# Kernel tuning notes

Measured on AMD Instinct MI355X. Metric: run time of the kernel, lower is better.

Reference implementation:

```python
import jax, jax.numpy as jnp
import numpy as np

B, N, IN, HD, NH, L, OUT = 256, 128, 9, 128, 8, 4, 60
DH = HD // NH
ALPHA = 0.6
EPS = 1e-5

def _ln(x, g, b):
    m = jnp.mean(x, axis=-1, keepdims=True)
    v = jnp.mean((x - m) ** 2, axis=-1, keepdims=True)
    return (x - m) * jax.lax.rsqrt(v + EPS) * g + b

def setup_inputs():
    key = jax.random.key(0)
    ks = jax.random.split(key, 30)
    p = lambda i, s: jax.random.normal(ks[i], s, jnp.float32) * 0.02
    strong = (jax.random.uniform(ks[25], (N, N)) < 0.15).astype(jnp.float32)
    strong = jnp.maximum(strong, jnp.eye(N, dtype=jnp.float32))  # self loops
    weak_mask = (jax.random.uniform(ks[26], (N, N)) < 0.10).astype(jnp.float32)
    return {
        'x': jax.random.normal(ks[0], (B, N, IN), jnp.float32),
        'conv_w': p(1, (HD, IN)), 'conv_b': p(2, (HD,)),
        'bn_gamma': jnp.ones((HD,), jnp.float32), 'bn_beta': jnp.zeros((HD,), jnp.float32),
        'bn_mean': jnp.zeros((HD,), jnp.float32), 'bn_var': jnp.ones((HD,), jnp.float32),
        'W': p(3, (L, HD, HD)), 'a_src': p(4, (L, NH, DH)), 'a_dst': p(5, (L, NH, DH)),
        'ln_g': jnp.ones((L, HD), jnp.float32), 'ln_b': jnp.zeros((L, HD), jnp.float32),
        'ffn_w1': p(6, (L, HD, 2 * HD)), 'ffn_b1': p(7, (L, 2 * HD)),
        'ffn_w2': p(8, (L, 2 * HD, HD)), 'ffn_b2': p(9, (L, HD)),
        'norm_g': jnp.ones((HD,), jnp.float32), 'norm_b': jnp.zeros((HD,), jnp.float32),
        'proj_w': p(10, (HD, HD)), 'proj_b': p(11, (HD,)),
        'head_w1': p(12, (HD, HD // 2)), 'head_b1': p(13, (HD // 2,)),
        'head_w2': p(14, (HD // 2, OUT)), 'head_b2': p(15, (OUT,)),
        'strong_adj': strong, 'weak_mask': weak_mask,
        'weak_param': p(16, (N, N)), 'edge_weight_adj': p(17, (N, N)),
    }

def reference(x, conv_w, conv_b, bn_gamma, bn_beta, bn_mean, bn_var, W, a_src, a_dst, ln_g, ln_b, ffn_w1, ffn_b1, ffn_w2, ffn_b2, norm_g, norm_b, proj_w, proj_b, head_w1, head_b1, head_w2, head_b2, strong_adj, weak_mask, weak_param, edge_weight_adj):
    # embedding: Conv1d(k=1) == per-node linear, then eval-mode BatchNorm1d + ReLU
    h = jnp.einsum('bni,oi->bno', x, conv_w) + conv_b  # [B,N,HD]
    h = (h - bn_mean) * jax.lax.rsqrt(bn_var + EPS) * bn_gamma + bn_beta
    h = jax.nn.relu(h)
    # weak adjacency: learnable gated edges, row-normalized (shared across layers)
    Aw = jax.nn.sigmoid(weak_param) * weak_mask
    Aw = Aw / (jnp.sum(Aw, axis=-1, keepdims=True) + EPS)  # [N,N]
    for i in range(L):
        res = h
        hp = jnp.einsum('bnd,de->bne', h, W[i]).reshape(B, N, NH, DH)
        s = jnp.einsum('bnhd,hd->bnh', hp, a_src[i])
        t = jnp.einsum('bnhd,hd->bnh', hp, a_dst[i])
        e = jax.nn.leaky_relu(s[:, :, None, :] + t[:, None, :, :], 0.2)  # [B,N,N,H]
        e = e + edge_weight_adj[None, :, :, None]  # learned per-edge bias
        e = jnp.where(strong_adj[None, :, :, None] > 0, e, jnp.float32(-1e9))
        att = jax.nn.softmax(e, axis=2)  # softmax over neighbors j
        strong_out = jnp.einsum('bijh,bjhd->bihd', att, hp)
        weak_out = jnp.einsum('ij,bjhd->bihd', Aw, hp)
        g = jax.nn.relu(ALPHA * strong_out + (1.0 - ALPHA) * weak_out).reshape(B, N, HD)
        g = _ln(g, ln_g[i], ln_b[i])
        g = jax.nn.relu(g @ ffn_w1[i] + ffn_b1[i]) @ ffn_w2[i] + ffn_b2[i]
        h = g + res
    h = _ln(h, norm_g, norm_b)
    h = h @ proj_w + proj_b
    h = jnp.mean(h, axis=1)  # mean-pool over nodes -> [B,HD]
    h = jax.nn.relu(h @ head_w1 + head_b1)
    return h @ head_w2 + head_b2  # [B,OUT]
```

## Files before the change

kernel.cpp:

```cpp
#include <hip/hip_runtime.h>
#include <hip/hip_bf16.h>

typedef __hip_bfloat16 bf16;
typedef unsigned short u16;
typedef __attribute__((ext_vector_type(8))) short bfrag;
typedef __attribute__((ext_vector_type(4))) float cfrag;

union BF { bfrag v; u16 u[8]; unsigned w[4]; };
union CF { cfrag v; float f[4]; };

#define MFMA(a,b,c) __builtin_amdgcn_mfma_f32_16x16x32_bf16(a,b,c,0,0,0)

#define BB   256
#define NN   128
#define IND  9
#define HDD  128
#define LLY  4
#define OUTD 60
#define LOG2E 1.44269504f
#define STR  136

__device__ __forceinline__ float b2f(bf16 v){ return __bfloat162float(v); }
__device__ __forceinline__ float u2f(u16 u){ return __uint_as_float(((unsigned)u) << 16); }
__device__ __forceinline__ u16 f2bf_bits(float f){
    unsigned u = __float_as_uint(f);
    return (u16)((u + 0x7FFFu + ((u >> 16) & 1u)) >> 16);
}
__device__ __forceinline__ unsigned pk2(float a, float b){
    union { __hip_bfloat162 h; unsigned u; } c;
    c.h = __float22bfloat162_rn(make_float2(a, b));
    return c.u;
}
__device__ __forceinline__ float wave_sum(float v){
    #pragma unroll
    for (int m = 32; m; m >>= 1) v += __shfl_xor(v, m, 64);
    return v;
}
__device__ __forceinline__ float ldin(const void* p, int i, bool isbf){
    return isbf ? b2f(((const bf16*)p)[i]) : ((const float*)p)[i];
}

struct SrcPtrs { const void* p[28]; };

__device__ const int NCV_OFF[19] = {0,1152,1280,1408,1536,1664,1792,2304,2816,3840,
                                    4352,4480,4608,20992,21120,29312,29376,33216,33276};
__device__ const int NCV_SRC[18] = {1,2,3,4,5,6,10,11,13,15,16,17,18,19,20,21,22,23};

__global__ __launch_bounds__(256) void k_prep(
    SrcPtrs S, float* __restrict__ pf,
    u16* __restrict__ WT, u16* __restrict__ w1T, u16* __restrict__ w2T,
    u16* __restrict__ WAb, u16* __restrict__ ew2, u16* __restrict__ Aw16,
    int* __restrict__ flagOut)
{
    __shared__ float tile[64][65];
    const unsigned* xw = (const unsigned*)S.p[0];
    int lane = threadIdx.x & 63;
    int cnt = 0;
    for (int i = lane; i < 512; i += 64) {
        float v = __uint_as_float((xw[i] & 0xFFFFu) << 16);
        if (!(fabsf(v) < 32.f)) cnt++;
    }
    bool isbf = wave_sum((float)cnt) < 16.f;
    if (blockIdx.x == 0 && threadIdx.x == 0) *flagOut = isbf ? 1 : 0;

    int blk = blockIdx.x, tid = threadIdx.x;
    if (blk < 131) {
        int idx = blk * 256 + tid;
        if (idx < 33276) {
            int y = 17;
            #pragma unroll 1
            for (int t = 1; t < 18; t++) if (idx < NCV_OFF[t]) { y = t - 1; break; }
            pf[idx] = ldin(S.p[NCV_SRC[y]], idx - NCV_OFF[y], isbf);
        }
    } else if (blk < 211) {
        const void* src; u16* dst; int K, N, k0, n0;
        if (blk < 147) {
            int t = blk - 131, l = t >> 2, tt = t & 3;
            src = (const char*)S.p[7] + (size_t)l * 16384 * (isbf ? 2 : 4);
            dst = WT + l * 16384; K = 128; N = 128; k0 = (tt >> 1) * 64; n0 = (tt & 1) * 64;
        } else if (blk < 179) {
            int t = blk - 147, l = t >> 3, tt = t & 7;
            src = (const char*)S.p[12] + (size_t)l * 32768 * (isbf ? 2 : 4);
            dst = w1T + l * 32768; K = 128; N = 256; k0 = (tt >> 2) * 64; n0 = (tt & 3) * 64;
        } else {
            int t = blk - 179, l = t >> 3, tt = t & 7;
            src = (const char*)S.p[14] + (size_t)l * 32768 * (isbf ? 2 : 4);
            dst = w2T + l * 32768; K = 256; N = 128; k0 = (tt & 3) * 64; n0 = (tt >> 2) * 64;
        }
        int ty = tid >> 6, tx = tid & 63;
        #pragma unroll 4
        for (int i = 0; i < 16; i++) {
            int row = ty * 16 + i;
            tile[row][tx] = ldin(src, (k0 + row) * N + n0 + tx, isbf);
        }
        __syncthreads();
        #pragma unroll 4
        for (int i = 0; i < 16; i++) {
            int row = ty * 16 + i;
            dst[(n0 + row) * K + k0 + tx] = f2bf_bits(tile[tx][row]);
        }
    } else if (blk < 243) {
        int j = (blk - 211) * 256 + tid;
        int l = j >> 11, r = j & 2047, n = r >> 7, k = r & 127;
        int h = n & 7;
        const void* ap = (n < 8) ? S.p[8] : S.p[9];
        float sacc = 0.f;
        #pragma unroll 1
        for (int d = 0; d < 16; d++)
            sacc += ldin(S.p[7], l * 16384 + k * 128 + h * 16 + d, isbf)
                  * ldin(ap, l * 128 + h * 16 + d, isbf);
        WAb[j] = f2bf_bits(sacc);
    } else if (blk < 307) {
        int j = (blk - 243) * 256 + tid;
        float sav = ldin(S.p[24], j, isbf);
        float ewv = ldin(S.p[27], j, isbf);
        ew2[j] = f2bf_bits(sav > 0.f ? ewv * LOG2E : -1e30f);
    } else {
        __shared__ float red[2];
        int i = blk - 307, j = tid & 127;
        float v = 0.f;
        if (tid < 128) {
            float wmv = ldin(S.p[25], i * 128 + j, isbf);
            float wpv = ldin(S.p[26], i * 128 + j, isbf);
            v = wmv / (1.f + __expf(-wpv));
            float sm = wave_sum(v);
            if ((tid & 63) == 0) red[tid >> 6] = sm;
        }
        __syncthreads();
        if (tid < 128) {
            float tot = red[0] + red[1];
            Aw16[i * 128 + j] = f2bf_bits(0.4f * v / (tot + 1e-5f));
        }
    }
}

#define LDSB (128*STR*2*2 + 128*132*4 + 2560*4)
__global__ __launch_bounds__(512, 2) void k_net(
    const void* __restrict__ xraw, const int* __restrict__ flag,
    const float* __restrict__ pf,
    const u16* __restrict__ WTg, const u16* __restrict__ WAbg,
    const u16* __restrict__ Awg, const u16* __restrict__ ew2g,
    const u16* __restrict__ w1Tg, const u16* __restrict__ w2Tg,
    void* __restrict__ outv)
{
    extern __shared__ __align__(16) char smem[];
    u16* U1 = (u16*)smem;
    u16* U2 = U1 + 128 * STR;
    float* hf32 = (float*)(U2 + 128 * STR);
    float* st2  = hf32 + 128 * 132;
    float* s2   = st2;
    u16*   t2u  = (u16*)(st2 + 1024);
    float* invb = st2 + 1536;

    const int b = blockIdx.x;
    const int tid = threadIdx.x, lane = tid & 63, wv = tid >> 6;
    const int l15 = lane & 15, kg = lane >> 4;
    const int wrow = wv * 16;
    const int arow = wrow + l15;
    const bool isbf = (*flag != 0);

    {
        float xr[4][IND];
        #pragma unroll
        for (int r = 0; r < 4; r++) {
            int bn = b * NN + wrow + kg * 4 + r;
            #pragma unroll
            for (int k = 0; k < IND; k++) xr[r][k] = ldin(xraw, bn * IND + k, isbf);
        }
        #pragma unroll 1
        for (int nt = 0; nt < 8; nt++) {
            int d = nt * 16 + l15;
            float cwreg[IND];
            #pragma unroll
            for (int k = 0; k < IND; k++) cwreg[k] = pf[d * IND + k];
            float scale = rsqrtf(pf[1664 + d] + 1e-5f) * pf[1280 + d];
            float bias  = pf[1408 + d] - pf[1536 + d] * scale;
            float cbd   = pf[1152 + d];
            #pragma unroll
            for (int r = 0; r < 4; r++) {
                float a = cbd;
                #pragma unroll
                for (int k = 0; k < IND; k++) a = fmaf(xr[r][k], cwreg[k], a);
                a = fmaxf(fmaf(a, scale, bias), 0.f);
                int row = wrow + kg * 4 + r;
                hf32[row * 132 + d] = a;
                U1[row * STR + d] = f2bf_bits(a);
            }
        }
    }

    #pragma unroll 1
    for (int l = 0; l < LLY; l++) {
        const u16* WT  = WTg  + l * 16384;
        const u16* WAb = WAbg + l * 2048;
        const u16* w1T = w1Tg + l * 32768;
        const u16* w2T = w2Tg + l * 32768;
        const float* fb1 = pf + 2816 + l * 256;
        const float* fb2 = pf + 3840 + l * 128;
        const float* lng = pf + 1792 + l * 128;
        const float* lnb = pf + 2304 + l * 128;

        __syncthreads();

        {
            CF acc[8], ast;
            #pragma unroll
            for (int r = 0; r < 4; r++) ast.f[r] = 0.f;
            #pragma unroll
            for (int nt = 0; nt < 8; nt++)
                #pragma unroll
                for (int r = 0; r < 4; r++) acc[nt].f[r] = 0.f;
            #pragma unroll
            for (int kk = 0; kk < 4; kk++) {
                bfrag af  = *(const bfrag*)&U1[arow * STR + kk*32 + kg*8];
                bfrag wab = *(const bfrag*)&WAb[l15 * 128 + kk*32 + kg*8];
                ast.v = MFMA(af, wab, ast.v);
                #pragma unroll
                for (int nt = 0; nt < 8; nt++) {
                    bfrag bw = *(const bfrag*)&WT[(nt*16 + l15) * 128 + kk*32 + kg*8];
                    acc[nt].v = MFMA(af, bw, acc[nt].v);
                }
            }
            #pragma unroll
            for (int nt = 0; nt < 8; nt++) {
                int col = nt*16 + l15;
                #pragma unroll
                for (int rp = 0; rp < 2; rp++) {
                    int row = wrow + kg*4 + rp*2;
                    *(unsigned*)&U2[col * STR + row] = pk2(acc[nt].f[rp*2], acc[nt].f[rp*2+1]);
                }
            }
            #pragma unroll
            for (int r = 0; r < 4; r++) {
                int node = wrow + kg*4 + r;
                float v = ast.f[r] * LOG2E;
                if (l15 < 8) s2[l15 * 128 + node] = v;
                else         t2u[(l15 - 8) * 128 + node] = f2bf_bits(v);
            }
        }
        __syncthreads();

        CF accS[8];
        #pragma unroll
        for (int nt = 0; nt < 8; nt++)
            #pragma unroll
            for (int r = 0; r < 4; r++) accS[nt].f[r] = 0.f;
        BF e2f[4];
        #pragma unroll
        for (int kk = 0; kk < 4; kk++)
            e2f[kk].v = *(const bfrag*)&ew2g[arow * 128 + kk*32 + kg*8];
        #pragma unroll 1
        for (int h = 0; h < 8; h++) {
            float sA = s2[h * 128 + arow];
            float sm = 0.f;
            #pragma unroll
            for (int kk = 0; kk < 4; kk++) {
                bfrag hb = *(const bfrag*)&U2[(h*16 + l15) * STR + kk*32 + kg*8];
                BF tb; tb.v = *(const bfrag*)&t2u[h * 128 + kk*32 + kg*8];
                BF pb;
                float p0[8];
                #pragma unroll
                for (int j = 0; j < 8; j++) {
                    float x2 = sA + u2f(tb.u[j]);
                    float lk = fmaxf(x2, 0.2f * x2);
                    float p = __builtin_amdgcn_exp2f(lk + u2f(e2f[kk].u[j]));
                    p0[j] = p; sm += p;
                }
                #pragma unroll
                for (int q = 0; q < 4; q++) pb.w[q] = pk2(p0[2*q], p0[2*q+1]);
                accS[h].v = MFMA(pb.v, hb, accS[h].v);
            }
            sm += __shfl_xor(sm, 16, 64);
            sm += __shfl_xor(sm, 32, 64);
            invb[h * 128 + arow] = 0.6f * __builtin_amdgcn_rcpf(sm);
        }
        #pragma unroll
        for (int h = 0; h < 8; h++) {
            const float4 iv = *(const float4*)&invb[h * 128 + wrow + kg*4];
            accS[h].f[0] *= iv.x; accS[h].f[1] *= iv.y;
            accS[h].f[2] *= iv.z; accS[h].f[3] *= iv.w;
        }

        #pragma unroll
        for (int kk = 0; kk < 4; kk++) {
            bfrag awf = *(const bfrag*)&Awg[arow * 128 + kk*32 + kg*8];
            #pragma unroll
            for (int nt = 0; nt < 8; nt++) {
                bfrag hb2 = *(const bfrag*)&U2[(nt*16 + l15) * STR + kk*32 + kg*8];
                accS[nt].v = MFMA(awf, hb2, accS[nt].v);
            }
        }

        #pragma unroll
        for (int r = 0; r < 4; r++) {
            float s1 = 0.f, sq = 0.f;
            #pragma unroll
            for (int nt = 0; nt < 8; nt++) {
                float x = fmaxf(accS[nt].f[r], 0.f);
                accS[nt].f[r] = x; s1 += x; sq = fmaf(x, x, sq);
            }
            #pragma unroll
            for (int m = 1; m <= 8; m <<= 1) { s1 += __shfl_xor(s1, m, 64); sq += __shfl_xor(sq, m, 64); }
            float mu = s1 * (1.f / 128.f);
            float var = sq * (1.f / 128.f) - mu * mu;
            float rs = rsqrtf(fmaxf(var, 0.f) + 1e-5f);
            #pragma unroll
            for (int nt = 0; nt < 8; nt++) {
                int col = nt*16 + l15;
                U1[(wrow + kg*4 + r) * STR + col] =
                    f2bf_bits(fmaf((accS[nt].f[r] - mu) * rs, lng[col], lnb[col]));
            }
        }

        __syncthreads();
        CF acc2[8];
        #pragma unroll
        for (int nt = 0; nt < 8; nt++)
            #pragma unroll
            for (int r = 0; r < 4; r++) acc2[nt].f[r] = 0.f;
        #pragma unroll 1
        for (int nh = 0; nh < 2; nh++) {
            CF a1[8];
            #pragma unroll
            for (int nt = 0; nt < 8; nt++)
                #pragma unroll
                for (int r = 0; r < 4; r++) a1[nt].f[r] = 0.f;
            #pragma unroll
            for (int kk = 0; kk < 4; kk++) {
                bfrag gf = *(const bfrag*)&U1[arow * STR + kk*32 + kg*8];
                #pragma unroll
                for (int nt = 0; nt < 8; nt++) {
                    bfrag wf = *(const bfrag*)&w1T[(nh*128 + nt*16 + l15) * 128 + kk*32 + kg*8];
                    a1[nt].v = MFMA(gf, wf, a1[nt].v);
                }
            }
            #pragma unroll
            for (int nt = 0; nt < 8; nt++) {
                int col = nt*16 + l15;
                float b1v = fb1[nh*128 + col];
                #pragma unroll
                for (int r = 0; r < 4; r++)
                    U2[(wrow + kg*4 + r) * STR + col] = f2bf_bits(fmaxf(a1[nt].f[r] + b1v, 0.f));
            }
            #pragma unroll
            for (int kk = 0; kk < 4; kk++) {
                bfrag hf = *(const bfrag*)&U2[arow * STR + kk*32 + kg*8];
                #pragma unroll
                for (int nt = 0; nt < 8; nt++) {
                    bfrag wf = *(const bfrag*)&w2T[(nt*16 + l15) * 256 + nh*128 + kk*32 + kg*8];
                    acc2[nt].v = MFMA(hf, wf, acc2[nt].v);
                }
            }
        }

        #pragma unroll
        for (int nt = 0; nt < 8; nt++) {
            int col = nt*16 + l15;
            float b2v = fb2[col];
            #pragma unroll
            for (int r = 0; r < 4; r++) {
                int row = wrow + kg*4 + r;
                float hv = hf32[row * 132 + col] + acc2[nt].f[r] + b2v;
                hf32[row * 132 + col] = hv;
                if (l < LLY - 1) U1[row * STR + col] = f2bf_bits(hv);
            }
        }
    }

    const float* ng = pf + 4352;
    const float* nb = pf + 4480;
    float pacc[8];
    #pragma unroll
    for (int nt = 0; nt < 8; nt++) pacc[nt] = 0.f;
    #pragma unroll
    for (int r = 0; r < 4; r++) {
        int row = wrow + kg*4 + r;
        float hvv[8];
        float s1 = 0.f, sq = 0.f;
        #pragma unroll
        for (int nt = 0; nt < 8; nt++) {
            float x = hf32[row * 132 + nt*16 + l15];
            hvv[nt] = x; s1 += x; sq = fmaf(x, x, sq);
        }
        #pragma unroll
        for (int m = 1; m <= 8; m <<= 1) { s1 += __shfl_xor(s1, m, 64); sq += __shfl_xor(sq, m, 64); }
        float mu = s1 * (1.f / 128.f);
        float var = sq * (1.f / 128.f) - mu * mu;
        float rs = rsqrtf(fmaxf(var, 0.f) + 1e-5f);
        #pragma unroll
        for (int nt = 0; nt < 8; nt++)
            pacc[nt] += fmaf((hvv[nt] - mu) * rs, ng[nt*16 + l15], nb[nt*16 + l15]);
    }
    #pragma unroll
    for (int nt = 0; nt < 8; nt++) {
        pacc[nt] += __shfl_xor(pacc[nt], 16, 64);
        pacc[nt] += __shfl_xor(pacc[nt], 32, 64);
    }
    __syncthreads();
    if (kg == 0) {
        #pragma unroll
        for (int nt = 0; nt < 8; nt++) st2[wv * 128 + nt*16 + l15] = pacc[nt];
    }
    __syncthreads();
    if (tid < 128) {
        float tot = 0.f;
        #pragma unroll
        for (int w = 0; w < 8; w++) tot += st2[w * 128 + tid];
        st2[1024 + tid] = tot * (1.f / 128.f);
    }
    __syncthreads();
    {
        int e = tid & 127, kq = tid >> 7;
        float a = 0.f;
        #pragma unroll 4
        for (int k = kq * 32; k < kq * 32 + 32; k++)
            a = fmaf(st2[1024 + k], pf[4608 + k * 128 + e], a);
        st2[1152 + kq * 128 + e] = a;
    }
    __syncthreads();
    if (tid < 128)
        st2[1664 + tid] = st2[1152 + tid] + st2[1280 + tid] + st2[1408 + tid] + st2[1536 + tid]
                        + pf[20992 + tid];
    __syncthreads();
    if (tid < 64) {
        float a1 = pf[29312 + tid];
        #pragma unroll 4
        for (int k = 0; k < 128; k++) a1 = fmaf(st2[1664 + k], pf[21120 + k * 64 + tid], a1);
        st2[1792 + tid] = fmaxf(a1, 0.f);
    }
    __syncthreads();
    if (tid < OUTD) {
        float a2 = pf[33216 + tid];
        #pragma unroll 4
        for (int k = 0; k < 64; k++) a2 = fmaf(st2[1792 + k], pf[29376 + k * OUTD + tid], a2);
        if (isbf) ((bf16*)outv)[b * OUTD + tid] = __float2bfloat16(a2);
        else      ((float*)outv)[b * OUTD + tid] = a2;
    }
}

extern "C" void kernel_launch(void* const* d_in, const int* in_sizes, int n_in,
                              void* d_out, int out_size, void* d_ws, size_t ws_size,
                              hipStream_t stream)
{
    float* ws = (float*)d_ws;
    float* pf = ws;
    int*   flag = (int*)(ws + 33280);
    u16* WT16   = (u16*)(ws + 33536);
    u16* w1T16  = WT16 + 65536;
    u16* w2T16  = w1T16 + 131072;
    u16* WAb16  = w2T16 + 131072;
    u16* Aw16   = WAb16 + 8192;
    u16* ew2p   = Aw16 + 16384;

    SrcPtrs S;
    for (int i = 0; i < 28; i++) S.p[i] = d_in[i];

    hipFuncSetAttribute((const void*)k_net,
                        hipFuncAttributeMaxDynamicSharedMemorySize, LDSB);

    k_prep<<<435, 256, 0, stream>>>(S, pf, WT16, w1T16, w2T16, WAb16, ew2p, Aw16, flag);
    k_net<<<BB, 512, LDSB, stream>>>(d_in[0], flag, pf,
                                     WT16, WAb16, Aw16, ew2p, w1T16, w2T16, d_out);
}
```

Measured before the change: 401.5 us.

## Split GEMMs into half-width passes and fold softmax normalization before MFMA

Splits the W projection and FFN first-layer GEMMs into two passes of four output tiles each, which reduces live accumulator registers. The weak-adjacency aggregation now runs before the attention loop. Each head's softmax probabilities are scaled by the reciprocal sum before the bf16 pack, which removes the invb LDS buffer and the per-head rescale pass. Launch bounds change from 2 blocks per CU to 1, so the compiler may use more registers, and scaling probabilities before bf16 conversion slightly changes rounding.

```diff
diff --git a/kernel.cpp b/kernel.cpp
--- a/kernel.cpp
+++ b/kernel.cpp
@@ -135,7 +135,7 @@
 }
 
 #define LDSB (128*STR*2*2 + 128*132*4 + 2560*4)
-__global__ __launch_bounds__(512, 2) void k_net(
+__global__ __launch_bounds__(512, 1) void k_net(
     const void* __restrict__ xraw, const int* __restrict__ flag,
     const float* __restrict__ pf,
     const u16* __restrict__ WTg, const u16* __restrict__ WAbg,
@@ -146,11 +146,10 @@
     extern __shared__ __align__(16) char smem[];
     u16* U1 = (u16*)smem;
     u16* U2 = U1 + 128 * STR;
-    float* hf32 = (float*)(U2 + 128 * STR);
-    float* st2  = hf32 + 128 * 132;
+    float* hres = (float*)(U2 + 128 * STR);
+    float* st2  = hres + 128 * 132;
     float* s2   = st2;
     u16*   t2u  = (u16*)(st2 + 1024);
-    float* invb = st2 + 1536;
 
     const int b = blockIdx.x;
     const int tid = threadIdx.x, lane = tid & 63, wv = tid >> 6;
@@ -183,7 +182,7 @@
                 for (int k = 0; k < IND; k++) a = fmaf(xr[r][k], cwreg[k], a);
                 a = fmaxf(fmaf(a, scale, bias), 0.f);
                 int row = wrow + kg * 4 + r;
-                hf32[row * 132 + d] = a;
+                hres[row * 132 + d] = a;
                 U1[row * STR + d] = f2bf_bits(a);
             }
         }
@@ -202,40 +201,45 @@
 
         __syncthreads();
 
-        {
-            CF acc[8], ast;
+        #pragma unroll 1
+        for (int pass = 0; pass < 2; pass++) {
+            CF acc[4], ast;
+            #pragma unroll
+            for (int q = 0; q < 4; q++)
+                #pragma unroll
+                for (int r = 0; r < 4; r++) acc[q].f[r] = 0.f;
             #pragma unroll
             for (int r = 0; r < 4; r++) ast.f[r] = 0.f;
             #pragma unroll
-            for (int nt = 0; nt < 8; nt++)
-                #pragma unroll
-                for (int r = 0; r < 4; r++) acc[nt].f[r] = 0.f;
-            #pragma unroll
             for (int kk = 0; kk < 4; kk++) {
-                bfrag af  = *(const bfrag*)&U1[arow * STR + kk*32 + kg*8];
-                bfrag wab = *(const bfrag*)&WAb[l15 * 128 + kk*32 + kg*8];
-                ast.v = MFMA(af, wab, ast.v);
-                #pragma unroll
-                for (int nt = 0; nt < 8; nt++) {
-                    bfrag bw = *(const bfrag*)&WT[(nt*16 + l15) * 128 + kk*32 + kg*8];
-                    acc[nt].v = MFMA(af, bw, acc[nt].v);
-                }
-            }
-            #pragma unroll
-            for (int nt = 0; nt < 8; nt++) {
-                int col = nt*16 + l15;
+                bfrag af = *(const bfrag*)&U1[arow * STR + kk*32 + kg*8];
+                if (pass == 0) {
+                    bfrag wab = *(const bfrag*)&WAb[l15 * 128 + kk*32 + kg*8];
+                    ast.v = MFMA(af, wab, ast.v);
+                }
+                #pragma unroll
+                for (int q = 0; q < 4; q++) {
+                    bfrag bw = *(const bfrag*)&WT[((pass*4+q)*16 + l15) * 128 + kk*32 + kg*8];
+                    acc[q].v = MFMA(af, bw, acc[q].v);
+                }
+            }
+            #pragma unroll
+            for (int q = 0; q < 4; q++) {
+                int col = (pass*4+q)*16 + l15;
                 #pragma unroll
                 for (int rp = 0; rp < 2; rp++) {
                     int row = wrow + kg*4 + rp*2;
-                    *(unsigned*)&U2[col * STR + row] = pk2(acc[nt].f[rp*2], acc[nt].f[rp*2+1]);
-                }
-            }
-            #pragma unroll
-            for (int r = 0; r < 4; r++) {
-                int node = wrow + kg*4 + r;
-                float v = ast.f[r] * LOG2E;
-                if (l15 < 8) s2[l15 * 128 + node] = v;
-                else         t2u[(l15 - 8) * 128 + node] = f2bf_bits(v);
+                    *(unsigned*)&U2[col * STR + row] = pk2(acc[q].f[rp*2], acc[q].f[rp*2+1]);
+                }
+            }
+            if (pass == 0) {
+                #pragma unroll
+                for (int r = 0; r < 4; r++) {
+                    int node = wrow + kg*4 + r;
+                    float v = ast.f[r] * LOG2E;
+                    if (l15 < 8) s2[l15 * 128 + node] = v;
+                    else         t2u[(l15 - 8) * 128 + node] = f2bf_bits(v);
+                }
             }
         }
         __syncthreads();
@@ -245,49 +249,54 @@
         for (int nt = 0; nt < 8; nt++)
             #pragma unroll
             for (int r = 0; r < 4; r++) accS[nt].f[r] = 0.f;
+        #pragma unroll 1
+        for (int pass = 0; pass < 2; pass++) {
+            #pragma unroll
+            for (int kk = 0; kk < 4; kk++) {
+                bfrag awf = *(const bfrag*)&Awg[arow * 128 + kk*32 + kg*8];
+                #pragma unroll
+                for (int q = 0; q < 4; q++) {
+                    int nt = pass*4 + q;
+                    bfrag hb2 = *(const bfrag*)&U2[(nt*16 + l15) * STR + kk*32 + kg*8];
+                    accS[nt].v = MFMA(awf, hb2, accS[nt].v);
+                }
+            }
+        }
+
         BF e2f[4];
         #pragma unroll
         for (int kk = 0; kk < 4; kk++)
             e2f[kk].v = *(const bfrag*)&ew2g[arow * 128 + kk*32 + kg*8];
         #pragma unroll 1
         for (int h = 0; h < 8; h++) {
+            bfrag hb[4];
+            #pragma unroll
+            for (int kk = 0; kk < 4; kk++)
+                hb[kk] = *(const bfrag*)&U2[(h*16 + l15) * STR + kk*32 + kg*8];
             float sA = s2[h * 128 + arow];
+            float pv[4][8];
             float sm = 0.f;
             #pragma unroll
             for (int kk = 0; kk < 4; kk++) {
-                bfrag hb = *(const bfrag*)&U2[(h*16 + l15) * STR + kk*32 + kg*8];
                 BF tb; tb.v = *(const bfrag*)&t2u[h * 128 + kk*32 + kg*8];
-                BF pb;
-                float p0[8];
                 #pragma unroll
                 for (int j = 0; j < 8; j++) {
                     float x2 = sA + u2f(tb.u[j]);
                     float lk = fmaxf(x2, 0.2f * x2);
                     float p = __builtin_amdgcn_exp2f(lk + u2f(e2f[kk].u[j]));
-                    p0[j] = p; sm += p;
-                }
-                #pragma unroll
-                for (int q = 0; q < 4; q++) pb.w[q] = pk2(p0[2*q], p0[2*q+1]);
-                accS[h].v = MFMA(pb.v, hb, accS[h].v);
+                    pv[kk][j] = p; sm += p;
+                }
             }
             sm += __shfl_xor(sm, 16, 64);
             sm += __shfl_xor(sm, 32, 64);
-            invb[h * 128 + arow] = 0.6f * __builtin_amdgcn_rcpf(sm);
-        }
-        #pragma unroll
-        for (int h = 0; h < 8; h++) {
-            const float4 iv = *(const float4*)&invb[h * 128 + wrow + kg*4];
-            accS[h].f[0] *= iv.x; accS[h].f[1] *= iv.y;
-            accS[h].f[2] *= iv.z; accS[h].f[3] *= iv.w;
-        }
-
-        #pragma unroll
-        for (int kk = 0; kk < 4; kk++) {
-            bfrag awf = *(const bfrag*)&Awg[arow * 128 + kk*32 + kg*8];
-            #pragma unroll
-            for (int nt = 0; nt < 8; nt++) {
-                bfrag hb2 = *(const bfrag*)&U2[(nt*16 + l15) * STR + kk*32 + kg*8];
-                accS[nt].v = MFMA(awf, hb2, accS[nt].v);
+            float sc = 0.6f * __builtin_amdgcn_rcpf(sm);
+            #pragma unroll
+            for (int kk = 0; kk < 4; kk++) {
+                BF pb;
+                #pragma unroll
+                for (int q = 0; q < 4; q++)
+                    pb.w[q] = pk2(pv[kk][2*q] * sc, pv[kk][2*q+1] * sc);
+                accS[h].v = MFMA(pb.v, hb[kk], accS[h].v);
             }
         }
 
@@ -313,6 +322,7 @@
         }
 
         __syncthreads();
+
         CF acc2[8];
         #pragma unroll
         for (int nt = 0; nt < 8; nt++)
@@ -320,27 +330,32 @@
             for (int r = 0; r < 4; r++) acc2[nt].f[r] = 0.f;
         #pragma unroll 1
         for (int nh = 0; nh < 2; nh++) {
-            CF a1[8];
-            #pragma unroll
-            for (int nt = 0; nt < 8; nt++)
-                #pragma unroll
-                for (int r = 0; r < 4; r++) a1[nt].f[r] = 0.f;
-            #pragma unroll
-            for (int kk = 0; kk < 4; kk++) {
-                bfrag gf = *(const bfrag*)&U1[arow * STR + kk*32 + kg*8];
-                #pragma unroll
-                for (int nt = 0; nt < 8; nt++) {
-                    bfrag wf = *(const bfrag*)&w1T[(nh*128 + nt*16 + l15) * 128 + kk*32 + kg*8];
-                    a1[nt].v = MFMA(gf, wf, a1[nt].v);
-                }
-            }
-            #pragma unroll
-            for (int nt = 0; nt < 8; nt++) {
-                int col = nt*16 + l15;
-                float b1v = fb1[nh*128 + col];
-                #pragma unroll
-                for (int r = 0; r < 4; r++)
-                    U2[(wrow + kg*4 + r) * STR + col] = f2bf_bits(fmaxf(a1[nt].f[r] + b1v, 0.f));
+            #pragma unroll 1
+            for (int pass = 0; pass < 2; pass++) {
+                CF a1[4];
+                #pragma unroll
+                for (int q = 0; q < 4; q++)
+                    #pragma unroll
+                    for (int r = 0; r < 4; r++) a1[q].f[r] = 0.f;
+                #pragma unroll
+                for (int kk = 0; kk < 4; kk++) {
+                    bfrag gf = *(const bfrag*)&U1[arow * STR + kk*32 + kg*8];
+                    #pragma unroll
+                    for (int q = 0; q < 4; q++) {
+                        int n = nh*128 + (pass*4+q)*16 + l15;
+                        bfrag wf = *(const bfrag*)&w1T[n * 128 + kk*32 + kg*8];
+                        a1[q].v = MFMA(gf, wf, a1[q].v);
+                    }
+                }
+                #pragma unroll
+                for (int q = 0; q < 4; q++) {
+                    int col = (pass*4+q)*16 + l15;
+                    float b1v = fb1[nh*128 + col];
+                    #pragma unroll
+                    for (int r = 0; r < 4; r++)
+                        U2[(wrow + kg*4 + r) * STR + col] =
+                            f2bf_bits(fmaxf(a1[q].f[r] + b1v, 0.f));
+                }
             }
             #pragma unroll
             for (int kk = 0; kk < 4; kk++) {
@@ -360,8 +375,8 @@
             #pragma unroll
             for (int r = 0; r < 4; r++) {
                 int row = wrow + kg*4 + r;
-                float hv = hf32[row * 132 + col] + acc2[nt].f[r] + b2v;
-                hf32[row * 132 + col] = hv;
+                float hv = hres[row * 132 + col] + acc2[nt].f[r] + b2v;
+                hres[row * 132 + col] = hv;
                 if (l < LLY - 1) U1[row * STR + col] = f2bf_bits(hv);
             }
         }
@@ -379,7 +394,7 @@
         float s1 = 0.f, sq = 0.f;
         #pragma unroll
         for (int nt = 0; nt < 8; nt++) {
-            float x = hf32[row * 132 + nt*16 + l15];
+            float x = hres[row * 132 + nt*16 + l15];
             hvv[nt] = x; s1 += x; sq = fmaf(x, x, sq);
         }
         #pragma unroll
```

Result: faster. 377.3 us (-6.0%).

## Fold softmax normalization into probabilities before MFMA and reorder weak aggregation

Applied to the files above, without the earlier changes.

The weak-adjacency MFMA now runs before the attention loop, and the softmax scale is applied to the probabilities before bf16 packing. This removes the LDS round trip through the invb buffer and the per-head rescaling pass. The head and FFN loops are fully unrolled, and launch bounds drop to one block per CU to allow more registers. The cost is higher register pressure and lower occupancy, plus a slightly different rounding order from scaling before packing.

```diff
diff --git a/kernel.cpp b/kernel.cpp
--- a/kernel.cpp
+++ b/kernel.cpp
@@ -135,7 +135,7 @@
 }
 
 #define LDSB (128*STR*2*2 + 128*132*4 + 2560*4)
-__global__ __launch_bounds__(512, 2) void k_net(
+__global__ __launch_bounds__(512, 1) void k_net(
     const void* __restrict__ xraw, const int* __restrict__ flag,
     const float* __restrict__ pf,
     const u16* __restrict__ WTg, const u16* __restrict__ WAbg,
@@ -146,11 +146,10 @@
     extern __shared__ __align__(16) char smem[];
     u16* U1 = (u16*)smem;
     u16* U2 = U1 + 128 * STR;
-    float* hf32 = (float*)(U2 + 128 * STR);
-    float* st2  = hf32 + 128 * 132;
+    float* hres = (float*)(U2 + 128 * STR);
+    float* st2  = hres + 128 * 132;
     float* s2   = st2;
     u16*   t2u  = (u16*)(st2 + 1024);
-    float* invb = st2 + 1536;
 
     const int b = blockIdx.x;
     const int tid = threadIdx.x, lane = tid & 63, wv = tid >> 6;
@@ -183,7 +182,7 @@
                 for (int k = 0; k < IND; k++) a = fmaf(xr[r][k], cwreg[k], a);
                 a = fmaxf(fmaf(a, scale, bias), 0.f);
                 int row = wrow + kg * 4 + r;
-                hf32[row * 132 + d] = a;
+                hres[row * 132 + d] = a;
                 U1[row * STR + d] = f2bf_bits(a);
             }
         }
@@ -245,49 +244,50 @@
         for (int nt = 0; nt < 8; nt++)
             #pragma unroll
             for (int r = 0; r < 4; r++) accS[nt].f[r] = 0.f;
+        #pragma unroll
+        for (int kk = 0; kk < 4; kk++) {
+            bfrag awf = *(const bfrag*)&Awg[arow * 128 + kk*32 + kg*8];
+            #pragma unroll
+            for (int nt = 0; nt < 8; nt++) {
+                bfrag hb2 = *(const bfrag*)&U2[(nt*16 + l15) * STR + kk*32 + kg*8];
+                accS[nt].v = MFMA(awf, hb2, accS[nt].v);
+            }
+        }
+
         BF e2f[4];
         #pragma unroll
         for (int kk = 0; kk < 4; kk++)
             e2f[kk].v = *(const bfrag*)&ew2g[arow * 128 + kk*32 + kg*8];
-        #pragma unroll 1
+        #pragma unroll
         for (int h = 0; h < 8; h++) {
+            bfrag hb[4];
+            #pragma unroll
+            for (int kk = 0; kk < 4; kk++)
+                hb[kk] = *(const bfrag*)&U2[(h*16 + l15) * STR + kk*32 + kg*8];
             float sA = s2[h * 128 + arow];
+            float pv[4][8];
             float sm = 0.f;
             #pragma unroll
             for (int kk = 0; kk < 4; kk++) {
-                bfrag hb = *(const bfrag*)&U2[(h*16 + l15) * STR + kk*32 + kg*8];
                 BF tb; tb.v = *(const bfrag*)&t2u[h * 128 + kk*32 + kg*8];
-                BF pb;
-                float p0[8];
                 #pragma unroll
                 for (int j = 0; j < 8; j++) {
                     float x2 = sA + u2f(tb.u[j]);
                     float lk = fmaxf(x2, 0.2f * x2);
                     float p = __builtin_amdgcn_exp2f(lk + u2f(e2f[kk].u[j]));
-                    p0[j] = p; sm += p;
+                    pv[kk][j] = p; sm += p;
                 }
-                #pragma unroll
-                for (int q = 0; q < 4; q++) pb.w[q] = pk2(p0[2*q], p0[2*q+1]);
-                accS[h].v = MFMA(pb.v, hb, accS[h].v);
             }
             sm += __shfl_xor(sm, 16, 64);
             sm += __shfl_xor(sm, 32, 64);
-            invb[h * 128 + arow] = 0.6f * __builtin_amdgcn_rcpf(sm);
-        }
-        #pragma unroll
-        for (int h = 0; h < 8; h++) {
-            const float4 iv = *(const float4*)&invb[h * 128 + wrow + kg*4];
-            accS[h].f[0] *= iv.x; accS[h].f[1] *= iv.y;
-            accS[h].f[2] *= iv.z; accS[h].f[3] *= iv.w;
-        }
-
-        #pragma unroll
-        for (int kk = 0; kk < 4; kk++) {
-            bfrag awf = *(const bfrag*)&Awg[arow * 128 + kk*32 + kg*8];
-            #pragma unroll
-            for (int nt = 0; nt < 8; nt++) {
-                bfrag hb2 = *(const bfrag*)&U2[(nt*16 + l15) * STR + kk*32 + kg*8];
-                accS[nt].v = MFMA(awf, hb2, accS[nt].v);
+            float sc = 0.6f * __builtin_amdgcn_rcpf(sm);
+            #pragma unroll
+            for (int kk = 0; kk < 4; kk++) {
+                BF pb;
+                #pragma unroll
+                for (int q = 0; q < 4; q++)
+                    pb.w[q] = pk2(pv[kk][2*q] * sc, pv[kk][2*q+1] * sc);
+                accS[h].v = MFMA(pb.v, hb[kk], accS[h].v);
             }
         }
 
@@ -313,12 +313,13 @@
         }
 
         __syncthreads();
+
         CF acc2[8];
         #pragma unroll
         for (int nt = 0; nt < 8; nt++)
             #pragma unroll
             for (int r = 0; r < 4; r++) acc2[nt].f[r] = 0.f;
-        #pragma unroll 1
+        #pragma unroll
         for (int nh = 0; nh < 2; nh++) {
             CF a1[8];
             #pragma unroll
@@ -360,8 +361,8 @@
             #pragma unroll
             for (int r = 0; r < 4; r++) {
                 int row = wrow + kg*4 + r;
-                float hv = hf32[row * 132 + col] + acc2[nt].f[r] + b2v;
-                hf32[row * 132 + col] = hv;
+                float hv = hres[row * 132 + col] + acc2[nt].f[r] + b2v;
+                hres[row * 132 + col] = hv;
                 if (l < LLY - 1) U1[row * STR + col] = f2bf_bits(hv);
             }
         }
@@ -379,7 +380,7 @@
         float s1 = 0.f, sq = 0.f;
         #pragma unroll
         for (int nt = 0; nt < 8; nt++) {
-            float x = hf32[row * 132 + nt*16 + l15];
+            float x = hres[row * 132 + nt*16 + l15];
             hvv[nt] = x; s1 += x; sq = fmaf(x, x, sq);
         }
         #pragma unroll
```

Measured after the change: 353.3 us. -12.0%, faster.
